# Optimization experiments

Measured on AMD Instinct MI355X. Metric: run time of the kernel, lower is better.

## Reference

```python
import jax, jax.numpy as jnp
import numpy as np

B, C, H, W = 4, 256, 128, 128
K = 3
BN = max(16, C // 4)  # 64
PAD = K // 2
EPS = 1e-5


def conv2d(x, w, b=None, pad=0):
    out = jax.lax.conv_general_dilated(
        x, w, (1, 1), [(pad, pad), (pad, pad)],
        dimension_numbers=("NCHW", "OIHW", "NCHW"))
    if b is not None:
        out = out + b[None, :, None, None]
    return out


def deform_conv2d(z, offset, mask, w, b):
    # torchvision modulated deform conv v2: offset [B,2*K*K,H,W] interleaved (dy,dx),
    # mask [B,K*K,H,W], kernel positions row-major, stride 1, pad PAD.
    Bz, Cb, Hz, Wz = z.shape
    K2 = K * K
    off = offset.reshape(Bz, K2, 2, Hz, Wz)
    ky, kx = jnp.meshgrid(jnp.arange(K), jnp.arange(K), indexing="ij")
    # sampling positions py/px: [B, K2, H, W]
    py = off[:, :, 0] + jnp.arange(Hz)[None, None, :, None] + (ky.reshape(K2) - PAD)[None, :, None, None]
    px = off[:, :, 1] + jnp.arange(Wz)[None, None, None, :] + (kx.reshape(K2) - PAD)[None, :, None, None]
    y0 = jnp.floor(py)
    x0 = jnp.floor(px)
    wy1 = py - y0  # frac weights
    wx1 = px - x0
    z_flat = z.reshape(Bz, Cb, Hz * Wz)

    def gather(yy, xx, wgt):
        valid = (yy >= 0) & (yy < Hz) & (xx >= 0) & (xx < Wz)
        yc = jnp.clip(yy, 0, Hz - 1).astype(jnp.int32)
        xc = jnp.clip(xx, 0, Wz - 1).astype(jnp.int32)
        idx = (yc * Wz + xc).reshape(Bz, K2 * Hz * Wz)
        g = jnp.take_along_axis(z_flat, idx[:, None, :], axis=2)  # [B, Cb, K2*H*W]
        g = g.reshape(Bz, Cb, K2, Hz, Wz)
        return g * (wgt * valid.astype(z.dtype))[:, None]

    val = (gather(y0, x0, (1 - wy1) * (1 - wx1))
           + gather(y0, x0 + 1, (1 - wy1) * wx1)
           + gather(y0 + 1, x0, wy1 * (1 - wx1))
           + gather(y0 + 1, x0 + 1, wy1 * wx1))
    val = val * mask[:, None]  # modulate: [B, Cb, K2, H, W]
    out = jnp.einsum("bckhw,ock->bohw", val, w.reshape(w.shape[0], Cb, K2))
    return out + b[None, :, None, None]


def setup_inputs() -> dict:
    key = jax.random.key(0)
    ks = jax.random.split(key, 11)
    s = 0.05
    return {
        "x": jax.random.normal(ks[0], (B, C, H, W), jnp.float32),
        "down_w": jax.random.normal(ks[1], (BN, C, 1, 1), jnp.float32) * s,
        "off_w": jax.random.normal(ks[2], (2 * K * K, BN, 3, 3), jnp.float32) * s,
        "off_b": jax.random.normal(ks[3], (2 * K * K,), jnp.float32) * s,
        "mask_w": jax.random.normal(ks[4], (K * K, BN, 3, 3), jnp.float32) * s,
        "mask_b": jax.random.normal(ks[5], (K * K,), jnp.float32) * s,
        "def_w": jax.random.normal(ks[6], (BN, BN, K, K), jnp.float32) * s,
        "def_b": jax.random.normal(ks[7], (BN,), jnp.float32) * s,
        "up_w": jax.random.normal(ks[8], (C, BN, 1, 1), jnp.float32) * s,
        "gamma": jnp.ones((C,), jnp.float32),
        "beta": jnp.zeros((C,), jnp.float32),
    }


def reference(x, down_w, off_w, off_b, mask_w, mask_b, def_w, def_b, up_w, gamma, beta):
    z = conv2d(x, down_w)                               # 1x1 down: [B, BN, H, W]
    offset = conv2d(z, off_w, off_b, pad=1)             # [B, 18, H, W]
    mask = jax.nn.sigmoid(conv2d(z, mask_w, mask_b, pad=1))  # [B, 9, H, W]
    z = deform_conv2d(z, offset, mask, def_w, def_b)    # [B, BN, H, W]
    z = conv2d(z, up_w)                                 # 1x1 up: [B, C, H, W]
    y = x + z
    # BatchNorm2d in training mode: batch statistics over (B, H, W), biased var
    mean = jnp.mean(y, axis=(0, 2, 3), keepdims=True)
    var = jnp.var(y, axis=(0, 2, 3), keepdims=True)
    yh = (y - mean) * jax.lax.rsqrt(var + EPS)
    yh = yh * gamma[None, :, None, None] + beta[None, :, None, None]
    return yh * jax.nn.sigmoid(yh)  # SiLU
```

## Files before the change

### kernel.cpp

```cpp
#include <hip/hip_runtime.h>
#include <hip/hip_bf16.h>


typedef __attribute__((ext_vector_type(8))) short bf16x8;
typedef __attribute__((ext_vector_type(4))) short bf16x4;
typedef __attribute__((ext_vector_type(4))) float f32x4;

#define HW   16384
#define CC   256
#define BNC  64

#define WS_STATS   0
#define WS_SS      131072
#define WS_FD      135168
#define WS_FOM     167936
#define WS_FDEF    204800
#define WS_FUP     278528
#define WS_ZBF     311296
#define WS_OM      8699904
#define WS_Z2      15777792

__device__ __forceinline__ short f2b(float f) {
    unsigned u = __float_as_uint(f);
    unsigned r = (u + 0x7FFFu + ((u >> 16) & 1u)) >> 16;
    return (short)r;
}
__device__ __forceinline__ float b2f(short s) {
    return __uint_as_float(((unsigned)(unsigned short)s) << 16);
}

__global__ void k_prep(const float* __restrict__ down_w, const float* __restrict__ off_w,
                       const float* __restrict__ mask_w, const float* __restrict__ def_w,
                       const float* __restrict__ up_w, char* __restrict__ ws) {
    int g = blockIdx.x * 256 + threadIdx.x;
    int row = g >> 6, lane = g & 63;
    if (row >= 172) return;
    int l15 = lane & 15, q = lane >> 4;
    short vals[8];
    short* dst;
    if (row < 32) {
        int nt = row >> 3, kk = row & 7;
        int n = nt * 16 + l15;
        for (int j = 0; j < 8; ++j) {
            int c = kk * 32 + q * 8 + j;
            vals[j] = f2b(down_w[n * 256 + c]);
        }
        dst = (short*)(ws + WS_FD) + row * 512 + lane * 8;
    } else if (row < 68) {
        int r = row - 32; int nt = r / 18, kk = r % 18;
        int n = nt * 16 + l15;
        for (int j = 0; j < 8; ++j) {
            int kap = kk * 32 + q * 8 + j; int k = kap >> 6, c = kap & 63;
            float v = 0.f;
            if (n < 18)      v = off_w[(n * 64 + c) * 9 + k];
            else if (n < 27) v = mask_w[((n - 18) * 64 + c) * 9 + k];
            vals[j] = f2b(v);
        }
        dst = (short*)(ws + WS_FOM) + r * 512 + lane * 8;
    } else if (row < 140) {
        int r = row - 68; int nt = r / 18, kk = r % 18;
        int n = nt * 16 + l15;
        int u = kk * 4 + q, k = u >> 3;
        for (int j = 0; j < 8; ++j) {
            int c = (u & 7) * 8 + j;
            vals[j] = f2b(def_w[(n * 64 + c) * 9 + k]);
        }
        dst = (short*)(ws + WS_FDEF) + r * 512 + lane * 8;
    } else {
        int r = row - 140; int nt = r >> 1, kk = r & 1;
        int o = nt * 16 + l15;
        for (int j = 0; j < 8; ++j) {
            int c = kk * 32 + q * 8 + j;
            vals[j] = f2b(up_w[o * 64 + c]);
        }
        dst = (short*)(ws + WS_FUP) + r * 512 + lane * 8;
    }
    for (int j = 0; j < 8; ++j) dst[j] = vals[j];
}

__global__ __launch_bounds__(256) void k_down(const float* __restrict__ x,
                                              const short* __restrict__ wfd,
                                              short* __restrict__ zbf) {
    __shared__ __align__(16) short xl[64 * 264];
    int blk = blockIdx.x;
    int b = blk >> 8;
    int hw0 = (blk & 255) * 64;
    int t = threadIdx.x;
    const float* xb = x + (size_t)b * CC * HW + hw0;
    int px = t & 63, w = t >> 6;
    for (int h = 0; h < 8; ++h) {
        int c0 = h * 32 + w * 8;
        bf16x8 pk;
        #pragma unroll
        for (int j = 0; j < 8; ++j)
            pk[j] = f2b(xb[(size_t)(c0 + j) * HW + px]);
        *(bf16x8*)(&xl[px * 264 + c0]) = pk;
    }
    __syncthreads();
    int lane = t & 63, wv = t >> 6;
    int l15 = lane & 15, q = lane >> 4;
    bf16x8 A[8];
    const short* xrow = &xl[(wv * 16 + l15) * 264];
    for (int kk = 0; kk < 8; ++kk)
        A[kk] = *(const bf16x8*)(xrow + kk * 32 + q * 8);
    const bf16x8* Bp = (const bf16x8*)wfd;
    size_t obase = ((size_t)b * HW + hw0 + wv * 16) * 64;
    for (int nt = 0; nt < 4; ++nt) {
        f32x4 acc = {0.f, 0.f, 0.f, 0.f};
        for (int kk = 0; kk < 8; ++kk) {
            bf16x8 Bf = Bp[(nt * 8 + kk) * 64 + lane];
            acc = __builtin_amdgcn_mfma_f32_16x16x32_bf16(A[kk], Bf, acc, 0, 0, 0);
        }
        int n = nt * 16 + l15;
        for (int r = 0; r < 4; ++r) {
            int prow = q * 4 + r;
            zbf[obase + (size_t)prow * 64 + n] = f2b(acc[r]);
        }
    }
}

__global__ __launch_bounds__(256) void k_offmask(const short* __restrict__ zbf,
                                                 const short* __restrict__ wfom,
                                                 const float* __restrict__ off_b,
                                                 const float* __restrict__ mask_b,
                                                 float* __restrict__ om) {
    int blk = blockIdx.x;
    int b = blk >> 8;
    int hw0 = (blk & 255) * 64;
    int y = hw0 >> 7, x0 = hw0 & 127;
    int t = threadIdx.x, lane = t & 63, wv = t >> 6;
    int l15 = lane & 15, q = lane >> 4;
    int xx0 = x0 + wv * 16 + l15;
    const short* zb = zbf + (size_t)b * HW * 64;
    f32x4 acc0 = {0, 0, 0, 0}, acc1 = {0, 0, 0, 0};
    const bf16x8* Bp = (const bf16x8*)wfom;
    for (int kk = 0; kk < 18; ++kk) {
        int k = kk >> 1;
        int yy = y + (k / 3) - 1;
        int xx = xx0 + (k % 3) - 1;
        int c0 = (kk & 1) * 32 + q * 8;
        bf16x8 A = {0, 0, 0, 0, 0, 0, 0, 0};
        if (yy >= 0 && yy < 128 && xx >= 0 && xx < 128)
            A = *(const bf16x8*)(zb + ((size_t)(yy * 128 + xx)) * 64 + c0);
        bf16x8 B0 = Bp[kk * 64 + lane];
        bf16x8 B1 = Bp[(18 + kk) * 64 + lane];
        acc0 = __builtin_amdgcn_mfma_f32_16x16x32_bf16(A, B0, acc0, 0, 0, 0);
        acc1 = __builtin_amdgcn_mfma_f32_16x16x32_bf16(A, B1, acc1, 0, 0, 0);
    }
    float* omb = om + ((size_t)b * HW + hw0 + wv * 16) * 27;
    for (int half = 0; half < 2; ++half) {
        f32x4 acc = half ? acc1 : acc0;
        int n = half * 16 + l15;
        if (n < 27) {
            for (int r = 0; r < 4; ++r) {
                int prow = q * 4 + r;
                float v = acc[r];
                if (n < 18) v += off_b[n];
                else { v += mask_b[n - 18]; v = 1.f / (1.f + __expf(-v)); }
                omb[prow * 27 + n] = v;
            }
        }
    }
}

__global__ __launch_bounds__(256) void k_deform(const short* __restrict__ zbf,
                                                const float* __restrict__ om,
                                                const short* __restrict__ wfdef,
                                                const float* __restrict__ def_b,
                                                short* __restrict__ z2) {
    __shared__ __align__(16) short ldsZ[121 * 64];
    __shared__ int4   pAi4[144];
    __shared__ float4 pAw4[144];
    __shared__ int    pAf[144];
    __shared__ __align__(16) short valA[18 * 64 * 8];
    int blk = blockIdx.x;
    int b = blk >> 10;
    int tile = blk & 1023;
    int yt = (tile >> 5) << 2, xt = (tile & 31) << 2;
    int sy0 = yt - 3; sy0 = sy0 < 0 ? 0 : (sy0 > 117 ? 117 : sy0);
    int sx0 = xt - 3; sx0 = sx0 < 0 ? 0 : (sx0 > 117 ? 117 : sx0);
    int t = threadIdx.x;
    const short* zbs = zbf + (size_t)b * HW * 64;
    for (int u = t; u < 968; u += 256) {
        int r = u / 88, rem = u - r * 88;
        int p = rem >> 3, cg = rem & 7;
        int gp = (sy0 + r) * 128 + sx0 + p;
        int lpix = r * 11 + p;
        int slot = (cg + lpix) & 7;
        *(int4*)(&ldsZ[lpix * 64 + slot * 8]) = *(const int4*)(zbs + (size_t)gp * 64 + cg * 8);
    }
    if (t < 144) {
        int px = t / 9, k = t % 9;
        int oy = yt + (px >> 2), ox = xt + (px & 3);
        const float* p = om + ((size_t)b * HW + oy * 128 + ox) * 27;
        float dy = p[2 * k], dx = p[2 * k + 1], m = p[18 + k];
        float py  = (float)oy + (float)(k / 3 - 1) + dy;
        float pxf = (float)ox + (float)(k % 3 - 1) + dx;
        float fy = floorf(py), fx = floorf(pxf);
        int iy = (int)fy, ix = (int)fx;
        float wy = py - fy, wx = pxf - fx;
        float ww[4] = { (1.f - wy) * (1.f - wx) * m, (1.f - wy) * wx * m,
                        wy * (1.f - wx) * m,          wy * wx * m };
        bool flg = (iy >= sy0) && (iy + 1 <= sy0 + 10) && (ix >= sx0) && (ix + 1 <= sx0 + 10);
        int ys[2] = {iy, iy + 1}, xs[2] = {ix, ix + 1};
        int   ri[4]; float rw[4];
        for (int ci = 0; ci < 4; ++ci) {
            int cy = ys[ci >> 1], cx = xs[ci & 1];
            if (flg) {
                int lp = (cy - sy0) * 11 + (cx - sx0);
                ri[ci] = (lp << 6) | (lp & 7);
                rw[ci] = ww[ci];
            } else {
                bool v = (cy >= 0 && cy < 128 && cx >= 0 && cx < 128);
                ri[ci] = v ? (cy * 128 + cx) * 64 : 0;
                rw[ci] = v ? ww[ci] : 0.f;
            }
        }
        pAi4[t] = make_int4(ri[0], ri[1], ri[2], ri[3]);
        pAw4[t] = make_float4(rw[0], rw[1], rw[2], rw[3]);
        pAf[t]  = flg ? 1 : 0;
    }
    __syncthreads();
    for (int it = 0; it < 5; ++it) {
        int s = t + it * 256;
        if (s < 1152) {
            int px = s & 15, u = s >> 4;
            int k = u >> 3, cg = u & 7;
            int task = px * 9 + k;
            int4   idx = pAi4[task];
            float4 wt  = pAw4[task];
            int    flg = pAf[task];
            int   ii[4] = { idx.x, idx.y, idx.z, idx.w };
            float wwt[4] = { wt.x, wt.y, wt.z, wt.w };
            int cgs = cg * 8;
            float acc[8] = {0.f, 0.f, 0.f, 0.f, 0.f, 0.f, 0.f, 0.f};
            #pragma unroll
            for (int ci = 0; ci < 4; ++ci) {
                float w = wwt[ci];
                int4 d;
                if (flg) {
                    int v = ii[ci];
                    d = *(const int4*)(&ldsZ[(v & ~63) + (((cg + (v & 7)) & 7) << 3)]);
                } else {
                    d = *(const int4*)(zbs + ii[ci] + cgs);
                }
                int dp[4] = { d.x, d.y, d.z, d.w };
                #pragma unroll
                for (int p = 0; p < 4; ++p) {
                    float lo = __uint_as_float((unsigned)dp[p] << 16);
                    float hi = __uint_as_float((unsigned)dp[p] & 0xffff0000u);
                    acc[2 * p]     += w * lo;
                    acc[2 * p + 1] += w * hi;
                }
            }
            bf16x8 out;
            #pragma unroll
            for (int j = 0; j < 8; ++j) out[j] = f2b(acc[j]);
            *(bf16x8*)(&valA[s * 8]) = out;
        }
    }
    __syncthreads();
    int lane = t & 63, wv = t >> 6;
    int l15 = lane & 15, q = lane >> 4;
    f32x4 acc = {0, 0, 0, 0};
    const bf16x8* Bp = (const bf16x8*)wfdef;
    const bf16x8* Ap = (const bf16x8*)valA;
    for (int kk = 0; kk < 18; ++kk) {
        bf16x8 A  = Ap[kk * 64 + lane];
        bf16x8 Bf = Bp[(wv * 18 + kk) * 64 + lane];
        acc = __builtin_amdgcn_mfma_f32_16x16x32_bf16(A, Bf, acc, 0, 0, 0);
    }
    int n = wv * 16 + l15;
    float bias = def_b[n];
    short* z2b = z2 + (size_t)b * HW * 64;
    for (int r = 0; r < 4; ++r) {
        int prow = q * 4 + r;
        int hw = (yt + (prow >> 2)) * 128 + xt + (prow & 3);
        z2b[(size_t)hw * 64 + n] = f2b(acc[r] + bias);
    }
}

__global__ __launch_bounds__(256) void k_up(const short* __restrict__ z2,
                                            const short* __restrict__ wfup,
                                            const float* __restrict__ x,
                                            float* __restrict__ yout,
                                            float* __restrict__ stats) {
    __shared__ __align__(16) short yl[256 * 70];
    int blk = blockIdx.x;
    int b = blk >> 8;
    int hw0 = (blk & 255) * 64;
    int t = threadIdx.x, lane = t & 63, wv = t >> 6;
    int l15 = lane & 15, q = lane >> 4;
    const short* z2b = z2 + ((size_t)b * HW + hw0 + wv * 16) * 64;
    bf16x8 A0 = *(const bf16x8*)(z2b + (size_t)l15 * 64 + q * 8);
    bf16x8 A1 = *(const bf16x8*)(z2b + (size_t)l15 * 64 + 32 + q * 8);
    const bf16x8* Bp = (const bf16x8*)wfup;
    for (int nt = 0; nt < 16; ++nt) {
        f32x4 acc = {0, 0, 0, 0};
        acc = __builtin_amdgcn_mfma_f32_16x16x32_bf16(A0, Bp[(nt * 2 + 0) * 64 + lane], acc, 0, 0, 0);
        acc = __builtin_amdgcn_mfma_f32_16x16x32_bf16(A1, Bp[(nt * 2 + 1) * 64 + lane], acc, 0, 0, 0);
        int o = nt * 16 + l15;
        bf16x4 pk;
        #pragma unroll
        for (int r = 0; r < 4; ++r) pk[r] = f2b(acc[r]);
        *(bf16x4*)(&yl[o * 70 + wv * 16 + q * 4]) = pk;
    }
    __syncthreads();
    int i16 = t & 15, og = t >> 4;
    int bucket = blk & 63;
    size_t base = (size_t)b * CC * HW + hw0 + (size_t)i16 * 4;
    #pragma unroll
    for (int i = 0; i < 16; ++i) {
        int o = og + 16 * i;
        size_t pb = base + (size_t)o * HW;
        float4 xv = *(const float4*)(x + pb);
        bf16x4 uv = *(const bf16x4*)(&yl[o * 70 + i16 * 4]);
        float v0 = b2f(uv[0]) + xv.x;
        float v1 = b2f(uv[1]) + xv.y;
        float v2 = b2f(uv[2]) + xv.z;
        float v3 = b2f(uv[3]) + xv.w;
        *(float4*)(yout + pb) = make_float4(v0, v1, v2, v3);
        float s  = v0 + v1 + v2 + v3;
        float s2 = v0 * v0 + v1 * v1 + v2 * v2 + v3 * v3;
        #pragma unroll
        for (int m = 8; m >= 1; m >>= 1) { s += __shfl_xor(s, m); s2 += __shfl_xor(s2, m); }
        if (i16 == 0) {
            atomicAdd(&stats[bucket * 512 + o], s);
            atomicAdd(&stats[bucket * 512 + 256 + o], s2);
        }
    }
}

__global__ void k_stats(const float* __restrict__ stats, const float* __restrict__ gamma,
                        const float* __restrict__ beta, float* __restrict__ ss) {
    int o = threadIdx.x;
    float s = 0.f, s2 = 0.f;
    for (int u = 0; u < 64; ++u) { s += stats[u * 512 + o]; s2 += stats[u * 512 + 256 + o]; }
    float mean = s * (1.f / 65536.f);
    float var  = s2 * (1.f / 65536.f) - mean * mean;
    float rs = rsqrtf(var + 1e-5f);
    float sc = gamma[o] * rs;
    ss[o]       = sc;
    ss[256 + o] = beta[o] - mean * sc;
}

__global__ __launch_bounds__(256) void k_bn(float* __restrict__ y, const float* __restrict__ ss) {
    int g = blockIdx.x * 256 + threadIdx.x;
    int o = (g >> 10) & 255;
    float sc = ss[o], sh = ss[256 + o];
    float4* p = (float4*)y + (size_t)g * 4;
    for (int i = 0; i < 4; ++i) {
        float4 v = p[i];
        float vf[4] = { v.x, v.y, v.z, v.w };
        for (int j = 0; j < 4; ++j) {
            float h = vf[j] * sc + sh;
            vf[j] = h / (1.f + __expf(-h));
        }
        p[i] = make_float4(vf[0], vf[1], vf[2], vf[3]);
    }
}

extern "C" void kernel_launch(void* const* d_in, const int* in_sizes, int n_in,
                              void* d_out, int out_size, void* d_ws, size_t ws_size,
                              hipStream_t stream) {
    const float* x      = (const float*)d_in[0];
    const float* down_w = (const float*)d_in[1];
    const float* off_w  = (const float*)d_in[2];
    const float* off_b  = (const float*)d_in[3];
    const float* mask_w = (const float*)d_in[4];
    const float* mask_b = (const float*)d_in[5];
    const float* def_w  = (const float*)d_in[6];
    const float* def_b  = (const float*)d_in[7];
    const float* up_w   = (const float*)d_in[8];
    const float* gamma  = (const float*)d_in[9];
    const float* beta   = (const float*)d_in[10];
    char* ws = (char*)d_ws;
    float* stats = (float*)(ws + WS_STATS);
    float* ss    = (float*)(ws + WS_SS);
    short* wfd   = (short*)(ws + WS_FD);
    short* wfom  = (short*)(ws + WS_FOM);
    short* wfdef = (short*)(ws + WS_FDEF);
    short* wfup  = (short*)(ws + WS_FUP);
    short* zbf   = (short*)(ws + WS_ZBF);
    float* om    = (float*)(ws + WS_OM);
    short* z2    = (short*)(ws + WS_Z2);
    float* y     = (float*)d_out;

    hipMemsetAsync(stats, 0, 64 * 512 * sizeof(float), stream);
    hipLaunchKernelGGL(k_prep,    dim3(43),   dim3(256), 0, stream, down_w, off_w, mask_w, def_w, up_w, ws);
    hipLaunchKernelGGL(k_down,    dim3(1024), dim3(256), 0, stream, x, wfd, zbf);
    hipLaunchKernelGGL(k_offmask, dim3(1024), dim3(256), 0, stream, zbf, wfom, off_b, mask_b, om);
    hipLaunchKernelGGL(k_deform,  dim3(4096), dim3(256), 0, stream, zbf, om, wfdef, def_b, z2);
    hipLaunchKernelGGL(k_up,      dim3(1024), dim3(256), 0, stream, z2, wfup, x, y, stats);
    hipLaunchKernelGGL(k_stats,   dim3(1),    dim3(256), 0, stream, stats, gamma, beta, ss);
    hipLaunchKernelGGL(k_bn,      dim3(4096), dim3(256), 0, stream, y, ss);
}
```

Measured before the change: 240.0 us.

## Fuse deformable conv with 1x1 up-projection, residual add and BN stats

Merges the deform kernel and the up-projection kernel into one. Each block now handles a 1x16 pixel strip instead of a 4x4 tile, so the residual add can use contiguous float4 reads of x. The deform output is kept in a swizzled shared-memory tile and fed straight into the up-projection MFMAs, which removes the z2 round trip through global memory and one kernel launch. In exchange the halo grows to 7x22 pixels, more LDS is used per block, and statistics go into 128 atomic buckets instead of 64.

```diff
diff --git a/kernel.cpp b/kernel.cpp
--- a/kernel.cpp
+++ b/kernel.cpp
@@ -11,14 +11,13 @@
 #define BNC  64
 
 #define WS_STATS   0
-#define WS_SS      131072
-#define WS_FD      135168
-#define WS_FOM     167936
-#define WS_FDEF    204800
-#define WS_FUP     278528
-#define WS_ZBF     311296
-#define WS_OM      8699904
-#define WS_Z2      15777792
+#define WS_SS      262144
+#define WS_FD      264192
+#define WS_FOM     296960
+#define WS_FDEF    333824
+#define WS_FUP     407552
+#define WS_ZBF     440320
+#define WS_OM      8828928
 
 __device__ __forceinline__ short f2b(float f) {
     unsigned u = __float_as_uint(f);
@@ -163,36 +162,40 @@
     }
 }
 
-__global__ __launch_bounds__(256) void k_deform(const short* __restrict__ zbf,
-                                                const float* __restrict__ om,
-                                                const short* __restrict__ wfdef,
-                                                const float* __restrict__ def_b,
-                                                short* __restrict__ z2) {
-    __shared__ __align__(16) short ldsZ[121 * 64];
-    __shared__ int4   pAi4[144];
-    __shared__ float4 pAw4[144];
-    __shared__ int    pAf[144];
-    __shared__ __align__(16) short valA[18 * 64 * 8];
+__global__ __launch_bounds__(256) void k_deform_up(
+        const short* __restrict__ zbf, const float* __restrict__ om,
+        const short* __restrict__ wfdef, const float* __restrict__ def_b,
+        const short* __restrict__ wfup, const float* __restrict__ x,
+        float* __restrict__ yout, float* __restrict__ stats) {
+    __shared__ __align__(16) short ldsZ[154 * 64];
+    __shared__ __align__(16) short valA[1152 * 8];
+    __shared__ __align__(16) char  uSm[5184];
+    int4*   pAi4 = (int4*)uSm;
+    float4* pAw4 = (float4*)(uSm + 2304);
+    int*    pAf  = (int*)(uSm + 4608);
+    short*  z2t  = (short*)uSm;
+
     int blk = blockIdx.x;
     int b = blk >> 10;
     int tile = blk & 1023;
-    int yt = (tile >> 5) << 2, xt = (tile & 31) << 2;
-    int sy0 = yt - 3; sy0 = sy0 < 0 ? 0 : (sy0 > 117 ? 117 : sy0);
-    int sx0 = xt - 3; sx0 = sx0 < 0 ? 0 : (sx0 > 117 ? 117 : sx0);
+    int oy = tile >> 3, xt = (tile & 7) << 4;
+    int hw0 = oy * 128 + xt;
+    int sy0 = oy - 3; sy0 = sy0 < 0 ? 0 : (sy0 > 121 ? 121 : sy0);
+    int sx0 = xt - 3; sx0 = sx0 < 0 ? 0 : (sx0 > 106 ? 106 : sx0);
     int t = threadIdx.x;
     const short* zbs = zbf + (size_t)b * HW * 64;
-    for (int u = t; u < 968; u += 256) {
-        int r = u / 88, rem = u - r * 88;
+    for (int u = t; u < 1232; u += 256) {
+        int r = u / 176, rem = u - r * 176;
         int p = rem >> 3, cg = rem & 7;
         int gp = (sy0 + r) * 128 + sx0 + p;
-        int lpix = r * 11 + p;
+        int lpix = r * 22 + p;
         int slot = (cg + lpix) & 7;
         *(int4*)(&ldsZ[lpix * 64 + slot * 8]) = *(const int4*)(zbs + (size_t)gp * 64 + cg * 8);
     }
     if (t < 144) {
         int px = t / 9, k = t % 9;
-        int oy = yt + (px >> 2), ox = xt + (px & 3);
-        const float* p = om + ((size_t)b * HW + oy * 128 + ox) * 27;
+        int ox = xt + px;
+        const float* p = om + ((size_t)b * HW + hw0 + px) * 27;
         float dy = p[2 * k], dx = p[2 * k + 1], m = p[18 + k];
         float py  = (float)oy + (float)(k / 3 - 1) + dy;
         float pxf = (float)ox + (float)(k % 3 - 1) + dx;
@@ -201,13 +204,13 @@
         float wy = py - fy, wx = pxf - fx;
         float ww[4] = { (1.f - wy) * (1.f - wx) * m, (1.f - wy) * wx * m,
                         wy * (1.f - wx) * m,          wy * wx * m };
-        bool flg = (iy >= sy0) && (iy + 1 <= sy0 + 10) && (ix >= sx0) && (ix + 1 <= sx0 + 10);
+        bool flg = (iy >= sy0) && (iy + 1 <= sy0 + 6) && (ix >= sx0) && (ix + 1 <= sx0 + 21);
         int ys[2] = {iy, iy + 1}, xs[2] = {ix, ix + 1};
         int   ri[4]; float rw[4];
         for (int ci = 0; ci < 4; ++ci) {
             int cy = ys[ci >> 1], cx = xs[ci & 1];
             if (flg) {
-                int lp = (cy - sy0) * 11 + (cx - sx0);
+                int lp = (cy - sy0) * 22 + (cx - sx0);
                 ri[ci] = (lp << 6) | (lp & 7);
                 rw[ci] = ww[ci];
             } else {
@@ -262,69 +265,47 @@
     __syncthreads();
     int lane = t & 63, wv = t >> 6;
     int l15 = lane & 15, q = lane >> 4;
-    f32x4 acc = {0, 0, 0, 0};
-    const bf16x8* Bp = (const bf16x8*)wfdef;
-    const bf16x8* Ap = (const bf16x8*)valA;
-    for (int kk = 0; kk < 18; ++kk) {
-        bf16x8 A  = Ap[kk * 64 + lane];
-        bf16x8 Bf = Bp[(wv * 18 + kk) * 64 + lane];
-        acc = __builtin_amdgcn_mfma_f32_16x16x32_bf16(A, Bf, acc, 0, 0, 0);
-    }
-    int n = wv * 16 + l15;
-    float bias = def_b[n];
-    short* z2b = z2 + (size_t)b * HW * 64;
-    for (int r = 0; r < 4; ++r) {
-        int prow = q * 4 + r;
-        int hw = (yt + (prow >> 2)) * 128 + xt + (prow & 3);
-        z2b[(size_t)hw * 64 + n] = f2b(acc[r] + bias);
-    }
-}
-
-__global__ __launch_bounds__(256) void k_up(const short* __restrict__ z2,
-                                            const short* __restrict__ wfup,
-                                            const float* __restrict__ x,
-                                            float* __restrict__ yout,
-                                            float* __restrict__ stats) {
-    __shared__ __align__(16) short yl[256 * 70];
-    int blk = blockIdx.x;
-    int b = blk >> 8;
-    int hw0 = (blk & 255) * 64;
-    int t = threadIdx.x, lane = t & 63, wv = t >> 6;
-    int l15 = lane & 15, q = lane >> 4;
-    const short* z2b = z2 + ((size_t)b * HW + hw0 + wv * 16) * 64;
-    bf16x8 A0 = *(const bf16x8*)(z2b + (size_t)l15 * 64 + q * 8);
-    bf16x8 A1 = *(const bf16x8*)(z2b + (size_t)l15 * 64 + 32 + q * 8);
-    const bf16x8* Bp = (const bf16x8*)wfup;
-    for (int nt = 0; nt < 16; ++nt) {
+    {
         f32x4 acc = {0, 0, 0, 0};
-        acc = __builtin_amdgcn_mfma_f32_16x16x32_bf16(A0, Bp[(nt * 2 + 0) * 64 + lane], acc, 0, 0, 0);
-        acc = __builtin_amdgcn_mfma_f32_16x16x32_bf16(A1, Bp[(nt * 2 + 1) * 64 + lane], acc, 0, 0, 0);
-        int o = nt * 16 + l15;
-        bf16x4 pk;
-        #pragma unroll
-        for (int r = 0; r < 4; ++r) pk[r] = f2b(acc[r]);
-        *(bf16x4*)(&yl[o * 70 + wv * 16 + q * 4]) = pk;
+        const bf16x8* Bp = (const bf16x8*)wfdef;
+        const bf16x8* Ap = (const bf16x8*)valA;
+        for (int kk = 0; kk < 18; ++kk) {
+            bf16x8 A  = Ap[kk * 64 + lane];
+            bf16x8 Bf = Bp[(wv * 18 + kk) * 64 + lane];
+            acc = __builtin_amdgcn_mfma_f32_16x16x32_bf16(A, Bf, acc, 0, 0, 0);
+        }
+        int n = wv * 16 + l15;
+        float bias = def_b[n];
+        for (int r = 0; r < 4; ++r) {
+            int prow = q * 4 + r;
+            z2t[prow * 64 + (n ^ ((prow & 7) << 3))] = f2b(acc[r] + bias);
+        }
     }
     __syncthreads();
-    int i16 = t & 15, og = t >> 4;
-    int bucket = blk & 63;
-    size_t base = (size_t)b * CC * HW + hw0 + (size_t)i16 * 4;
-    #pragma unroll
-    for (int i = 0; i < 16; ++i) {
-        int o = og + 16 * i;
-        size_t pb = base + (size_t)o * HW;
+    int rsw = (l15 & 7) << 3;
+    bf16x8 A0 = *(const bf16x8*)&z2t[l15 * 64 + ((q * 8) ^ rsw)];
+    bf16x8 A1 = *(const bf16x8*)&z2t[l15 * 64 + ((32 + q * 8) ^ rsw)];
+    const bf16x8* Bu = (const bf16x8*)wfup;
+    int bucket = blk & 127;
+    size_t xybase = (size_t)b * CC * HW + hw0 + q * 4;
+    for (int nt = 0; nt < 4; ++nt) {
+        int ont = wv * 4 + nt;
+        f32x4 acc = {0, 0, 0, 0};
+        acc = __builtin_amdgcn_mfma_f32_16x16x32_bf16(A0, Bu[(ont * 2 + 0) * 64 + lane], acc, 0, 0, 0);
+        acc = __builtin_amdgcn_mfma_f32_16x16x32_bf16(A1, Bu[(ont * 2 + 1) * 64 + lane], acc, 0, 0, 0);
+        int o = ont * 16 + l15;
+        size_t pb = xybase + (size_t)o * HW;
         float4 xv = *(const float4*)(x + pb);
-        bf16x4 uv = *(const bf16x4*)(&yl[o * 70 + i16 * 4]);
-        float v0 = b2f(uv[0]) + xv.x;
-        float v1 = b2f(uv[1]) + xv.y;
-        float v2 = b2f(uv[2]) + xv.z;
-        float v3 = b2f(uv[3]) + xv.w;
+        float v0 = acc[0] + xv.x;
+        float v1 = acc[1] + xv.y;
+        float v2 = acc[2] + xv.z;
+        float v3 = acc[3] + xv.w;
         *(float4*)(yout + pb) = make_float4(v0, v1, v2, v3);
         float s  = v0 + v1 + v2 + v3;
         float s2 = v0 * v0 + v1 * v1 + v2 * v2 + v3 * v3;
-        #pragma unroll
-        for (int m = 8; m >= 1; m >>= 1) { s += __shfl_xor(s, m); s2 += __shfl_xor(s2, m); }
-        if (i16 == 0) {
+        s  += __shfl_xor(s, 16);  s  += __shfl_xor(s, 32);
+        s2 += __shfl_xor(s2, 16); s2 += __shfl_xor(s2, 32);
+        if (q == 0) {
             atomicAdd(&stats[bucket * 512 + o], s);
             atomicAdd(&stats[bucket * 512 + 256 + o], s2);
         }
@@ -335,7 +316,7 @@
                         const float* __restrict__ beta, float* __restrict__ ss) {
     int o = threadIdx.x;
     float s = 0.f, s2 = 0.f;
-    for (int u = 0; u < 64; ++u) { s += stats[u * 512 + o]; s2 += stats[u * 512 + 256 + o]; }
+    for (int u = 0; u < 128; ++u) { s += stats[u * 512 + o]; s2 += stats[u * 512 + 256 + o]; }
     float mean = s * (1.f / 65536.f);
     float var  = s2 * (1.f / 65536.f) - mean * mean;
     float rs = rsqrtf(var + 1e-5f);
@@ -383,15 +364,13 @@
     short* wfup  = (short*)(ws + WS_FUP);
     short* zbf   = (short*)(ws + WS_ZBF);
     float* om    = (float*)(ws + WS_OM);
-    short* z2    = (short*)(ws + WS_Z2);
     float* y     = (float*)d_out;
 
-    hipMemsetAsync(stats, 0, 64 * 512 * sizeof(float), stream);
-    hipLaunchKernelGGL(k_prep,    dim3(43),   dim3(256), 0, stream, down_w, off_w, mask_w, def_w, up_w, ws);
-    hipLaunchKernelGGL(k_down,    dim3(1024), dim3(256), 0, stream, x, wfd, zbf);
-    hipLaunchKernelGGL(k_offmask, dim3(1024), dim3(256), 0, stream, zbf, wfom, off_b, mask_b, om);
-    hipLaunchKernelGGL(k_deform,  dim3(4096), dim3(256), 0, stream, zbf, om, wfdef, def_b, z2);
-    hipLaunchKernelGGL(k_up,      dim3(1024), dim3(256), 0, stream, z2, wfup, x, y, stats);
-    hipLaunchKernelGGL(k_stats,   dim3(1),    dim3(256), 0, stream, stats, gamma, beta, ss);
-    hipLaunchKernelGGL(k_bn,      dim3(4096), dim3(256), 0, stream, y, ss);
-}
+    hipMemsetAsync(stats, 0, 128 * 512 * sizeof(float), stream);
+    hipLaunchKernelGGL(k_prep,      dim3(43),   dim3(256), 0, stream, down_w, off_w, mask_w, def_w, up_w, ws);
+    hipLaunchKernelGGL(k_down,      dim3(1024), dim3(256), 0, stream, x, wfd, zbf);
+    hipLaunchKernelGGL(k_offmask,   dim3(1024), dim3(256), 0, stream, zbf, wfom, off_b, mask_b, om);
+    hipLaunchKernelGGL(k_deform_up, dim3(4096), dim3(256), 0, stream, zbf, om, wfdef, def_b, wfup, x, y, stats);
+    hipLaunchKernelGGL(k_stats,     dim3(1),    dim3(256), 0, stream, stats, gamma, beta, ss);
+    hipLaunchKernelGGL(k_bn,        dim3(4096), dim3(256), 0, stream, y, ss);
+}
```

New measurement: 244.8 us. No clear change (+2.0%).
